# Performance work log

Hardware: AMD Instinct MI355X
Metric: run time of the kernel (lower is better)

## Reference

```python
import jax, jax.numpy as jnp
import numpy as np

D_MODEL = 4096
D_HIDDEN = 32768
BATCH = 2048
K = 128
N_DEAD = 2048


def _ln(x, eps=1e-5):
    # torch .std() is unbiased (ddof=1)
    mu = jnp.mean(x, axis=-1, keepdims=True)
    xc = x - mu
    std = jnp.std(x, axis=-1, keepdims=True, ddof=1)
    return xc / (std + eps), mu, std


def _topk_activation(x, k):
    # topk over last dim, relu values, scatter back into zeros
    vals, idx = jax.lax.top_k(x, k)          # [B, k]
    vals = jax.nn.relu(vals)
    rows = jnp.arange(x.shape[0])[:, None]    # [B, 1]
    return jnp.zeros_like(x).at[rows, idx].set(vals)


def setup_inputs() -> dict:
    key = jax.random.key(0)
    k1, k2 = jax.random.split(key)
    x = jax.random.normal(k1, (BATCH, D_MODEL), dtype=jnp.float32)
    # kaiming-uniform-ish encoder init
    bound = 1.0 / np.sqrt(D_MODEL)
    w_enc = jax.random.uniform(k2, (D_MODEL, D_HIDDEN), dtype=jnp.float32,
                               minval=-bound, maxval=bound)
    w_dec = w_enc.T
    w_dec = w_dec / jnp.linalg.norm(w_dec, axis=0, keepdims=True)
    b_enc = jnp.zeros((D_HIDDEN,), dtype=jnp.float32)
    b_pre = jnp.zeros((D_MODEL,), dtype=jnp.float32)
    # fixed dead-neuron mask with exactly N_DEAD dead latents
    dm = np.zeros((D_HIDDEN,), dtype=bool)
    rng = np.random.default_rng(0)
    dm[rng.choice(D_HIDDEN, size=N_DEAD, replace=False)] = True
    dead_mask = jnp.asarray(dm)
    return {"x": x, "w_enc": w_enc, "w_dec": w_dec, "b_enc": b_enc,
            "b_pre": b_pre, "dead_mask": dead_mask, "num_dead": N_DEAD}


def reference(x, w_enc, w_dec, b_enc, b_pre, dead_mask, num_dead):
    xn, mu, std = _ln(x)
    xc = xn - b_pre
    pre_acts = xc @ w_enc + b_enc                 # [B, d_hidden]
    latents = _topk_activation(pre_acts, K)
    recons = latents @ w_dec + b_pre              # [B, d_model]
    recons = recons * std + mu
    # auxk dead-neuron path (num_dead is a static python int)
    k_aux = min(x.shape[-1] // 2, num_dead)
    auxk_latents = jnp.where(dead_mask[None, :], pre_acts, -jnp.inf)
    auxk_acts = _topk_activation(auxk_latents, k_aux)
    auxk = auxk_acts @ w_dec + b_pre
    auxk = auxk * std + mu
    return recons, auxk, num_dead
```

## Files before the change

kernel.cpp:

```cpp
#include <hip/hip_runtime.h>
#include <math.h>

#define D_MODEL  4096
#define D_HIDDEN 32768
#define BATCH    2048
#define KSEL     128
#define NDEAD    2048
#define TIECAP   256

typedef short s16x8 __attribute__((ext_vector_type(8)));
typedef float f32x4 __attribute__((ext_vector_type(4)));

__device__ __forceinline__ unsigned int fkey(float f) {
    unsigned int u = __float_as_uint(f);
    return (u & 0x80000000u) ? ~u : (u | 0x80000000u);
}
__device__ __forceinline__ unsigned short f2bf(float f) {
    unsigned int u = __float_as_uint(f);
    u += 0x7FFFu + ((u >> 16) & 1u);
    return (unsigned short)(u >> 16);
}
__device__ __forceinline__ float bf2f(unsigned short h) {
    return __uint_as_float(((unsigned int)h) << 16);
}
__device__ __forceinline__ unsigned int key16x2(unsigned int u) {
    const unsigned int s = (u >> 15) & 0x10001u;
    const unsigned int mask = s * 0xFFFFu;
    return (u ^ mask) | (~mask & 0x80008000u);
}
__device__ __forceinline__ float unkey16(unsigned int k) {
    const unsigned int u = (k & 0x8000u) ? (k & 0x7FFFu) : (~k & 0xFFFFu);
    return __uint_as_float(u << 16);
}
__device__ __forceinline__ void async_copy16(void* lds_dst, const void* gsrc) {
    __builtin_amdgcn_global_load_lds(
        (const __attribute__((address_space(1))) unsigned int*)gsrc,
        (__attribute__((address_space(3))) unsigned int*)lds_dst,
        16, 0, 0);
}

__global__ __launch_bounds__(256) void ln_kernel(const float* __restrict__ x,
        double* __restrict__ mu, double* __restrict__ stdv, double* __restrict__ sinv)
{
    const int row = blockIdx.x;
    const int tid = threadIdx.x;
    const float* xr = x + (size_t)row * D_MODEL;
    float xv[16];
#pragma unroll
    for (int i = 0; i < 16; ++i) xv[i] = xr[tid + 256 * i];
    double s = 0.0;
#pragma unroll
    for (int i = 0; i < 16; ++i) s += (double)xv[i];
    __shared__ double red[4];
    __shared__ double sh_mu;
    const int lane = tid & 63, wid = tid >> 6;
#pragma unroll
    for (int off = 32; off > 0; off >>= 1) s += __shfl_down(s, off, 64);
    if (lane == 0) red[wid] = s;
    __syncthreads();
    if (tid == 0) sh_mu = (red[0] + red[1] + red[2] + red[3]) / (double)D_MODEL;
    __syncthreads();
    const double m = sh_mu;
    double s2 = 0.0;
#pragma unroll
    for (int i = 0; i < 16; ++i) { double d = (double)xv[i] - m; s2 += d * d; }
#pragma unroll
    for (int off = 32; off > 0; off >>= 1) s2 += __shfl_down(s2, off, 64);
    __syncthreads();
    if (lane == 0) red[wid] = s2;
    __syncthreads();
    if (tid == 0) {
        double var = (red[0] + red[1] + red[2] + red[3]) / (double)(D_MODEL - 1);
        double sd = sqrt(var);
        mu[row] = m;
        stdv[row] = sd;
        sinv[row] = 1.0 / (sd + 1e-5);
    }
}

__global__ void dead_scan_kernel(const unsigned char* __restrict__ mask8,
                                 int* __restrict__ dead_idx, int* __restrict__ dead_cnt,
                                 const int* __restrict__ num_dead_in, float* __restrict__ out_last)
{
    const int lane = threadIdx.x;
    int c = 0;
    for (int j = lane; j < D_HIDDEN; j += 64) c += (mask8[j] != 0);
#pragma unroll
    for (int off = 32; off > 0; off >>= 1) c += __shfl_down(c, off, 64);
    const int total_u8 = __shfl(c, 0, 64);
    const bool u8mode = (total_u8 == NDEAD);
    const int* mask32 = (const int*)mask8;
    int cnt = 0;
    for (int base = 0; base < D_HIDDEN; base += 64) {
        const int j = base + lane;
        const bool d = u8mode ? (mask8[j] != 0) : (mask32[j] != 0);
        const unsigned long long b = __ballot(d);
        const int pre = __popcll(b & ((1ull << lane) - 1ull));
        if (d && (cnt + pre) < NDEAD) dead_idx[cnt + pre] = j;
        cnt += __popcll(b);
    }
    const int cc = cnt > NDEAD ? NDEAD : cnt;
    if (lane == 0) {
        *dead_cnt = cc;
        *out_last = (float)(*num_dead_in);
    }
    for (int t = cc + lane; t < NDEAD; t += 64) dead_idx[t] = 0;
}

__global__ __launch_bounds__(256) void asplit_kernel(
    const float* __restrict__ x, const double* __restrict__ mu, const double* __restrict__ sinv,
    const float* __restrict__ b_pre, unsigned short* __restrict__ Ahp)
{
    const int row = blockIdx.x, tid = threadIdx.x;
    const double m = mu[row], si = sinv[row];
    const float* xr = x + (size_t)row * D_MODEL;
#pragma unroll
    for (int i = 0; i < 4; ++i) {
        const int j = (i * 256 + tid) * 4;
        const float4 xv = *(const float4*)(xr + j);
        const float4 bp = *(const float4*)(b_pre + j);
        float v[4];
        v[0] = (float)(((double)xv.x - m) * si) - bp.x;
        v[1] = (float)(((double)xv.y - m) * si) - bp.y;
        v[2] = (float)(((double)xv.z - m) * si) - bp.z;
        v[3] = (float)(((double)xv.w - m) * si) - bp.w;
        uint2 hw;
        hw.x = (unsigned)f2bf(v[0]) | ((unsigned)f2bf(v[1]) << 16);
        hw.y = (unsigned)f2bf(v[2]) | ((unsigned)f2bf(v[3]) << 16);
        *(uint2*)(Ahp + (size_t)row * D_MODEL + j) = hw;
    }
}

__global__ __launch_bounds__(256) void bsplit_kernel(
    const float* __restrict__ w_enc, unsigned short* __restrict__ Bhp)
{
    __shared__ float t[32][33];
    const int bk = blockIdx.x * 32;
    const int bn = blockIdx.y * 32;
    const int tid = threadIdx.x;
    const int lr = tid >> 3, lc4 = (tid & 7) * 4;
    const float4 v = *(const float4*)(w_enc + (size_t)(bk + lr) * D_HIDDEN + bn + lc4);
    t[lr][lc4 + 0] = v.x; t[lr][lc4 + 1] = v.y; t[lr][lc4 + 2] = v.z; t[lr][lc4 + 3] = v.w;
    __syncthreads();
    float o[4];
#pragma unroll
    for (int j = 0; j < 4; ++j) o[j] = t[lc4 + j][lr];
    uint2 hw;
    hw.x = (unsigned)f2bf(o[0]) | ((unsigned)f2bf(o[1]) << 16);
    hw.y = (unsigned)f2bf(o[2]) | ((unsigned)f2bf(o[3]) << 16);
    *(uint2*)(Bhp + (size_t)(bn + lr) * D_MODEL + bk + lc4) = hw;
}

__global__ __launch_bounds__(256) void wencT_kernel(
    const float* __restrict__ w_enc, float* __restrict__ wT)
{
    __shared__ float t[32][33];
    const int bk = blockIdx.x * 32;
    const int bn = blockIdx.y * 32;
    const int tid = threadIdx.x;
    const int lr = tid >> 3, lc4 = (tid & 7) * 4;
    const float4 v = *(const float4*)(w_enc + (size_t)(bk + lr) * D_HIDDEN + bn + lc4);
    t[lr][lc4 + 0] = v.x; t[lr][lc4 + 1] = v.y; t[lr][lc4 + 2] = v.z; t[lr][lc4 + 3] = v.w;
    __syncthreads();
    const int j = tid >> 3, i4 = (tid & 7) * 4;
    float4 o;
    o.x = t[i4 + 0][j]; o.y = t[i4 + 1][j]; o.z = t[i4 + 2][j]; o.w = t[i4 + 3][j];
    *(float4*)(wT + (size_t)(bn + j) * D_MODEL + bk + i4) = o;
}

template<int EPI>
__global__ __launch_bounds__(512) void mm256_kernel(
    const unsigned short* __restrict__ A, const unsigned short* __restrict__ B,
    const int kdim, const int ntiles_x,
    const float* __restrict__ bias_n,
    const double* __restrict__ muv, const double* __restrict__ stdvv,
    void* __restrict__ outp, const long ostride)
{
    __shared__ unsigned short lds[2 * 4 * 8192];
    const int tid = threadIdx.x;
    const int lane = tid & 63, wid = tid >> 6;
    const int cpx = gridDim.x >> 3;
    const int orig = blockIdx.x;
    const int wg = (orig & 7) * cpx + (orig >> 3);
    const int m0 = (wg % ntiles_x) * 256;
    const int n0 = (wg / ntiles_x) * 256;
    const int wm = (wid >> 2) * 128;
    const int wn = (wid & 3) * 64;
    const int fr = lane & 15, kq = lane >> 4;
    const int swr = (fr >> 1) & 3;
    const int qg = (lane & 3) ^ ((lane >> 3) & 3);
    const int qo = (kq ^ swr) * 8;

    f32x4 acc[8][4];
#pragma unroll
    for (int i = 0; i < 8; ++i)
#pragma unroll
        for (int j = 0; j < 4; ++j) acc[i][j] = (f32x4){0.f, 0.f, 0.f, 0.f};

    const unsigned short* srcs[8];
    int d0[8];
#pragma unroll
    for (int j = 0; j < 8; ++j) {
        const int s = wid * 8 + j;
        const int sp = s >> 4, sr = s & 15;
        const unsigned short* gp = (sp < 2) ? A : B;
        const int t0 = (sp < 2) ? m0 : n0;
        const int row = sr * 16 + (lane >> 2);
        srcs[j] = gp + (size_t)(t0 + row) * kdim + (sp & 1) * 32 + qg * 8;
        d0[j] = sp * 8192 + sr * 512;
    }

    const int NT = kdim >> 6;
#pragma unroll
    for (int j = 0; j < 8; ++j) async_copy16(lds + d0[j], srcs[j]);

    for (int t = 0; t < NT; ++t) {
        const int cur = t & 1;
        if (t + 1 < NT) {
            const int k1 = (t + 1) << 6;
#pragma unroll
            for (int j = 0; j < 8; ++j)
                async_copy16(lds + (cur ^ 1) * 32768 + d0[j], srcs[j] + k1);
            asm volatile("s_waitcnt vmcnt(8)" ::: "memory");
        } else {
            asm volatile("s_waitcnt vmcnt(0)" ::: "memory");
        }
        __builtin_amdgcn_s_barrier();
        __builtin_amdgcn_sched_barrier(0);

        const unsigned short* bb = lds + cur * 32768;
#pragma unroll
        for (int kk = 0; kk < 2; ++kk) {
            s16x8 a[8], b[4];
#pragma unroll
            for (int mi = 0; mi < 8; ++mi)
                a[mi] = *(const s16x8*)(bb + kk * 8192 + (wm + mi * 16 + fr) * 32 + qo);
#pragma unroll
            for (int ni = 0; ni < 4; ++ni)
                b[ni] = *(const s16x8*)(bb + (2 + kk) * 8192 + (wn + ni * 16 + fr) * 32 + qo);
            __builtin_amdgcn_s_setprio(1);
#pragma unroll
            for (int mi = 0; mi < 8; ++mi)
#pragma unroll
                for (int ni = 0; ni < 4; ++ni)
                    acc[mi][ni] = __builtin_amdgcn_mfma_f32_16x16x32_bf16(a[mi], b[ni], acc[mi][ni], 0, 0, 0);
            __builtin_amdgcn_s_setprio(0);
        }
        __builtin_amdgcn_sched_barrier(0);
        __builtin_amdgcn_s_barrier();
        __builtin_amdgcn_sched_barrier(0);
    }

#pragma unroll
    for (int ni = 0; ni < 4; ++ni) {
        const int col = n0 + wn + ni * 16 + fr;
        const float be = bias_n[col];
#pragma unroll
        for (int mi = 0; mi < 8; ++mi) {
            const int rb = m0 + wm + mi * 16 + kq * 4;
            if (EPI == 0) {
                unsigned short* O = (unsigned short*)outp;
#pragma unroll
                for (int r = 0; r < 4; ++r)
                    O[(size_t)(rb + r) * ostride + col] = f2bf(acc[mi][ni][r] + be);
            } else {
                float* O = (float*)outp;
#pragma unroll
                for (int r = 0; r < 4; ++r) {
                    const int m = rb + r;
                    O[(size_t)m * ostride + col] =
                        (acc[mi][ni][r] + be) * (float)stdvv[m] + (float)muv[m];
                }
            }
        }
    }
}

template<int EPI>
__global__ __launch_bounds__(256) void mm_kernel(
    const unsigned short* __restrict__ A, const unsigned short* __restrict__ B,
    const int kdim, const int ntiles_x,
    const float* __restrict__ bias_n,
    const double* __restrict__ muv, const double* __restrict__ stdvv,
    void* __restrict__ outp, const long ostride)
{
    __shared__ unsigned short lds[3 * 2 * 128 * 32];
    const int tid = threadIdx.x;
    const int lane = tid & 63, wid = tid >> 6;
    const int cpx = gridDim.x >> 3;
    const int orig = blockIdx.x;
    const int wg = (orig & 7) * cpx + (orig >> 3);
    const int m0 = (wg % ntiles_x) * 128;
    const int n0 = (wg / ntiles_x) * 128;
    const int wm = (wid >> 1) * 64, wn = (wid & 1) * 64;
    const int fr = lane & 15, kq = lane >> 4;
    const int swr = (fr >> 1) & 3;
    const int qg = (lane & 3) ^ ((lane >> 3) & 3);
    const int qo = (kq ^ swr) * 8;

    f32x4 acc[4][4];
#pragma unroll
    for (int i = 0; i < 4; ++i)
#pragma unroll
        for (int j = 0; j < 4; ++j) acc[i][j] = (f32x4){0.f, 0.f, 0.f, 0.f};

    const unsigned short* srcs[4];
    int d0[4];
#pragma unroll
    for (int j = 0; j < 4; ++j) {
        const int s = wid * 4 + j;
        const int pl = s >> 3, sr = s & 7;
        const int r = sr * 16 + (lane >> 2);
        srcs[j] = (pl ? B : A) + (size_t)((pl ? n0 : m0) + r) * kdim + qg * 8;
        d0[j] = pl * 4096 + sr * 512;
    }

    const int NT = kdim >> 5;
#pragma unroll
    for (int j = 0; j < 4; ++j) async_copy16(lds + 0 * 8192 + d0[j], srcs[j]);
#pragma unroll
    for (int j = 0; j < 4; ++j) async_copy16(lds + 1 * 8192 + d0[j], srcs[j] + 32);

    int cur = 0, nxt = 2;
    for (int t = 0; t < NT; ++t) {
        if (t < NT - 1) {
            asm volatile("s_waitcnt vmcnt(4)" ::: "memory");
        } else {
            asm volatile("s_waitcnt vmcnt(0)" ::: "memory");
        }
        __builtin_amdgcn_s_barrier();
        __builtin_amdgcn_sched_barrier(0);

        if (t + 2 < NT) {
            const int k2 = (t + 2) << 5;
#pragma unroll
            for (int j = 0; j < 4; ++j) async_copy16(lds + nxt * 8192 + d0[j], srcs[j] + k2);
        }

        const unsigned short* la = lds + cur * 8192;
        const unsigned short* lb = la + 4096;
        s16x8 a[4], b[4];
#pragma unroll
        for (int i = 0; i < 4; ++i) {
            a[i] = *(const s16x8*)(la + (wm + i * 16 + fr) * 32 + qo);
            b[i] = *(const s16x8*)(lb + (wn + i * 16 + fr) * 32 + qo);
        }
#pragma unroll
        for (int mi = 0; mi < 4; ++mi)
#pragma unroll
            for (int ni = 0; ni < 4; ++ni)
                acc[mi][ni] = __builtin_amdgcn_mfma_f32_16x16x32_bf16(a[mi], b[ni], acc[mi][ni], 0, 0, 0);

        cur = cur == 2 ? 0 : cur + 1;
        nxt = nxt == 2 ? 0 : nxt + 1;
    }

#pragma unroll
    for (int ni = 0; ni < 4; ++ni) {
        const int col = n0 + wn + ni * 16 + fr;
        const float be = bias_n[col];
#pragma unroll
        for (int mi = 0; mi < 4; ++mi) {
            const int rb = m0 + wm + mi * 16 + kq * 4;
            if (EPI == 0) {
                unsigned short* O = (unsigned short*)outp;
#pragma unroll
                for (int r = 0; r < 4; ++r)
                    O[(size_t)(rb + r) * ostride + col] = f2bf(acc[mi][ni][r] + be);
            } else {
                float* O = (float*)outp;
#pragma unroll
                for (int r = 0; r < 4; ++r) {
                    const int m = rb + r;
                    O[(size_t)m * ostride + col] =
                        (acc[mi][ni][r] + be) * (float)stdvv[m] + (float)muv[m];
                }
            }
        }
    }
}

__global__ __launch_bounds__(256) void topk_sel_kernel(
    const unsigned short* __restrict__ p16,
    int* __restrict__ topk_idx, float* __restrict__ topk_val,
    int* __restrict__ sure_cnt, int* __restrict__ tie_cnt, int* __restrict__ cand_col)
{
    const int row = blockIdx.x;
    const int tid = threadIdx.x;
    const int lane = tid & 63, wid = tid >> 6;
    const unsigned short* pr = p16 + (size_t)row * D_HIDDEN;

    __shared__ int red[4];
    __shared__ int sh_sel, sh_tie;

    uint4 kr[16];
#pragma unroll
    for (int i = 0; i < 16; ++i) {
        uint4 w = *(const uint4*)(pr + (i * 256 + tid) * 8);
        w.x = key16x2(w.x); w.y = key16x2(w.y); w.z = key16x2(w.z); w.w = key16x2(w.w);
        kr[i] = w;
    }
    if (tid == 0) { sh_sel = 0; sh_tie = 0; }

    unsigned int lo = 0, hi = 65535;
    while (lo < hi) {
        const unsigned int mid = (lo + hi) >> 1;
        int c = 0;
#pragma unroll
        for (int i = 0; i < 16; ++i) {
            const unsigned int u[4] = {kr[i].x, kr[i].y, kr[i].z, kr[i].w};
#pragma unroll
            for (int e = 0; e < 4; ++e) {
                c += (int)((u[e] & 0xFFFFu) > mid);
                c += (int)((u[e] >> 16) > mid);
            }
        }
#pragma unroll
        for (int off = 32; off > 0; off >>= 1) c += __shfl_down(c, off, 64);
        if (lane == 0) red[wid] = c;
        __syncthreads();
        const int total = red[0] + red[1] + red[2] + red[3];
        if (total < KSEL) hi = mid; else lo = mid + 1;
        __syncthreads();
    }
    const unsigned int K16 = lo;

    const float vc = unkey16(K16);
    const float DLT = 1.3e-2f;
    const float sureT = vc + 2.f * DLT;
    const float candT = vc - 2.f * DLT;
    const unsigned int sK = fkey(sureT) >> 16;
    const unsigned int cK = fkey(candT) >> 16;

    int* oidx = topk_idx + row * KSEL;
    float* oval = topk_val + row * KSEL;
    int* cc = cand_col + row * TIECAP;
#pragma unroll
    for (int i = 0; i < 16; ++i) {
        const int j0 = (i * 256 + tid) * 8;
        const unsigned int u[4] = {kr[i].x, kr[i].y, kr[i].z, kr[i].w};
#pragma unroll
        for (int e = 0; e < 8; ++e) {
            const unsigned int k = (e & 1) ? (u[e >> 1] >> 16) : (u[e >> 1] & 0xFFFFu);
            if (k < cK) continue;
            const float v = unkey16(k);
            if (k > sK && v > sureT) {
                const int pos = atomicAdd(&sh_sel, 1);
                oidx[pos] = j0 + e;
                oval[pos] = v > 0.f ? v : 0.f;
            } else if (v >= candT) {
                const int t = atomicAdd(&sh_tie, 1);
                if (t < TIECAP) cc[t] = j0 + e;
            }
        }
    }
    __syncthreads();
    if (tid == 0) {
        sure_cnt[row] = sh_sel;
        tie_cnt[row] = sh_tie > TIECAP ? TIECAP : sh_tie;
    }
}

__global__ __launch_bounds__(256) void topk_refine_kernel(
    const int* __restrict__ tie_cnt, const int* __restrict__ cand_col,
    double* __restrict__ cand_val,
    const float* __restrict__ x, const double* __restrict__ mu, const double* __restrict__ sinv,
    const float* __restrict__ b_pre, const float* __restrict__ wT, const float* __restrict__ b_enc)
{
    const int row = blockIdx.x;
    const int tid = threadIdx.x;
    const int lane = tid & 63, wid = tid >> 6;
    const int T = tie_cnt[row];
    const int base = (int)blockIdx.y * 4 + wid;
    if (base >= T) return;
    const double m_ = mu[row], si = sinv[row];
    const float* xr = x + (size_t)row * D_MODEL;
    for (int slot = base; slot < T; slot += 64) {
        const int col = cand_col[row * TIECAP + slot];
        const float* wr = wT + (size_t)col * D_MODEL;
        double s0 = 0.0, s1 = 0.0;
        for (int k = lane * 4; k < D_MODEL; k += 512) {
            {
                const float4 xv = *(const float4*)(xr + k);
                const float4 bp = *(const float4*)(b_pre + k);
                const float4 wv4 = *(const float4*)(wr + k);
                s0 += (((double)xv.x - m_) * si - (double)bp.x) * (double)wv4.x;
                s0 += (((double)xv.y - m_) * si - (double)bp.y) * (double)wv4.y;
                s0 += (((double)xv.z - m_) * si - (double)bp.z) * (double)wv4.z;
                s0 += (((double)xv.w - m_) * si - (double)bp.w) * (double)wv4.w;
            }
            {
                const int k2 = k + 256;
                const float4 xv = *(const float4*)(xr + k2);
                const float4 bp = *(const float4*)(b_pre + k2);
                const float4 wv4 = *(const float4*)(wr + k2);
                s1 += (((double)xv.x - m_) * si - (double)bp.x) * (double)wv4.x;
                s1 += (((double)xv.y - m_) * si - (double)bp.y) * (double)wv4.y;
                s1 += (((double)xv.z - m_) * si - (double)bp.z) * (double)wv4.z;
                s1 += (((double)xv.w - m_) * si - (double)bp.w) * (double)wv4.w;
            }
        }
        double s = s0 + s1;
#pragma unroll
        for (int off = 32; off > 0; off >>= 1) s += __shfl_down(s, off, 64);
        if (lane == 0) cand_val[row * TIECAP + slot] = s + (double)b_enc[col];
    }
}

__global__ __launch_bounds__(256) void topk_fin_kernel(
    const int* __restrict__ sure_cnt, const int* __restrict__ tie_cnt,
    const int* __restrict__ cand_col, const double* __restrict__ cand_val,
    int* __restrict__ topk_idx, float* __restrict__ topk_val)
{
    const int row = blockIdx.x;
    const int tid = threadIdx.x;
    __shared__ double vals[TIECAP];
    __shared__ int cols[TIECAP];
    const int G = sure_cnt[row];
    const int T = tie_cnt[row];
    const int R = KSEL - G;
    if (tid < T) {
        vals[tid] = cand_val[row * TIECAP + tid];
        cols[tid] = cand_col[row * TIECAP + tid];
    }
    __syncthreads();
    int* oidx = topk_idx + row * KSEL;
    float* oval = topk_val + row * KSEL;
    if (tid < T) {
        const double v = vals[tid];
        const int c = cols[tid];
        int rank = 0;
        for (int u = 0; u < T; ++u) {
            const double vu = vals[u];
            rank += (int)((vu > v) || (vu == v && cols[u] < c));
        }
        if (rank < R) {
            oidx[G + rank] = c;
            oval[G + rank] = v > 0.0 ? (float)v : 0.f;
        }
    }
    const int take = R < T ? R : T;
    if (tid >= take && tid < R) {
        oidx[G + tid] = (T > 0) ? cols[0] : 0;
        oval[G + tid] = 0.f;
    }
}

__global__ __launch_bounds__(256) void wdec2bf_kernel(
    const float* __restrict__ w_dec, unsigned short* __restrict__ wd16)
{
    const size_t gid = (size_t)blockIdx.x * 256 + threadIdx.x;
    const size_t base = gid * 8;
    const float4 a = *(const float4*)(w_dec + base);
    const float4 b = *(const float4*)(w_dec + base + 4);
    uint4 o;
    o.x = (unsigned)f2bf(a.x) | ((unsigned)f2bf(a.y) << 16);
    o.y = (unsigned)f2bf(a.z) | ((unsigned)f2bf(a.w) << 16);
    o.z = (unsigned)f2bf(b.x) | ((unsigned)f2bf(b.y) << 16);
    o.w = (unsigned)f2bf(b.z) | ((unsigned)f2bf(b.w) << 16);
    *(uint4*)(wd16 + base) = o;
}

__global__ __launch_bounds__(256) void decode_kernel(
    const int* __restrict__ topk_idx, const float* __restrict__ topk_val,
    const unsigned short* __restrict__ wd16, const float* __restrict__ b_pre,
    const double* __restrict__ mu, const double* __restrict__ stdv,
    float* __restrict__ out0)
{
    const int row = blockIdx.x;
    const int tid = threadIdx.x;
    __shared__ int sidx[KSEL];
    __shared__ float sval[KSEL];
    if (tid < KSEL) {
        sidx[tid] = topk_idx[row * KSEL + tid];
        sval[tid] = topk_val[row * KSEL + tid];
    }
    __syncthreads();
    float acc[16];
#pragma unroll
    for (int i = 0; i < 16; ++i) acc[i] = 0.f;
    const int dbase = tid * 16;
    for (int k = 0; k < KSEL; ++k) {
        const float v = sval[k];
        if (v == 0.f) continue;
        const uint4* wr = (const uint4*)(wd16 + (size_t)sidx[k] * D_MODEL + dbase);
        const uint4 w0 = wr[0], w1 = wr[1];
        const unsigned int u[8] = {w0.x, w0.y, w0.z, w0.w, w1.x, w1.y, w1.z, w1.w};
#pragma unroll
        for (int i = 0; i < 8; ++i) {
            acc[2 * i]     += v * __uint_as_float(u[i] << 16);
            acc[2 * i + 1] += v * __uint_as_float(u[i] & 0xFFFF0000u);
        }
    }
    const float st = (float)stdv[row];
    const float mm = (float)mu[row];
    float* o = out0 + (size_t)row * D_MODEL + dbase;
#pragma unroll
    for (int i = 0; i < 16; ++i) {
        o[i] = (acc[i] + b_pre[dbase + i]) * st + mm;
    }
}

__global__ __launch_bounds__(256) void auxg_kernel(
    const unsigned short* __restrict__ p16, const int* __restrict__ dead_idx,
    const int* __restrict__ dead_cnt, unsigned short* __restrict__ Ahd)
{
    const int r = blockIdx.x;
    const int tid = threadIdx.x;
    const int dc = *dead_cnt;
#pragma unroll
    for (int i = 0; i < 8; ++i) {
        const int c = i * 256 + tid;
        unsigned short v = 0;
        if (c < dc) {
            const unsigned short u = p16[(size_t)r * D_HIDDEN + dead_idx[c]];
            v = (u & 0x8000u) ? (unsigned short)0 : u;
        }
        Ahd[(size_t)r * NDEAD + c] = v;
    }
}

__global__ __launch_bounds__(256) void auxb_kernel(
    const float* __restrict__ w_dec, const int* __restrict__ dead_idx,
    unsigned short* __restrict__ Bhd)
{
    __shared__ float t[32][33];
    const int k0 = blockIdx.x * 32;
    const int n0 = blockIdx.y * 32;
    const int tid = threadIdx.x;
    const int i = tid >> 3, j4 = (tid & 7) * 4;
    const int srow = dead_idx[k0 + i];
    const float4 v = *(const float4*)(w_dec + (size_t)srow * D_MODEL + n0 + j4);
    t[i][j4 + 0] = v.x; t[i][j4 + 1] = v.y; t[i][j4 + 2] = v.z; t[i][j4 + 3] = v.w;
    __syncthreads();
    const int j = tid >> 3, i4 = (tid & 7) * 4;
    uint2 hw;
    hw.x = (unsigned)f2bf(t[i4 + 0][j]) | ((unsigned)f2bf(t[i4 + 1][j]) << 16);
    hw.y = (unsigned)f2bf(t[i4 + 2][j]) | ((unsigned)f2bf(t[i4 + 3][j]) << 16);
    *(uint2*)(Bhd + (size_t)(n0 + j) * NDEAD + k0 + i4) = hw;
}

extern "C" void kernel_launch(void* const* d_in, const int* in_sizes, int n_in,
                              void* d_out, int out_size, void* d_ws, size_t ws_size,
                              hipStream_t stream)
{
    (void)in_sizes; (void)n_in; (void)out_size; (void)ws_size;
    const float* x      = (const float*)d_in[0];
    const float* w_enc  = (const float*)d_in[1];
    const float* w_dec  = (const float*)d_in[2];
    const float* b_enc  = (const float*)d_in[3];
    const float* b_pre  = (const float*)d_in[4];
    const unsigned char* dead_mask = (const unsigned char*)d_in[5];
    const int* num_dead = (const int*)d_in[6];
    float* out = (float*)d_out;

    char* base = (char*)d_ws;
    char* w = base;
    auto alloc = [&](size_t bytes) -> char* {
        char* p = w;
        w += (bytes + 255) & ~(size_t)255;
        return p;
    };
    unsigned short* p16 = (unsigned short*)alloc((size_t)BATCH * D_HIDDEN * 2);
    double* mu       = (double*)alloc((size_t)BATCH * 8);
    double* stdv     = (double*)alloc((size_t)BATCH * 8);
    double* sinv     = (double*)alloc((size_t)BATCH * 8);
    int* topk_idx    = (int*)alloc((size_t)BATCH * KSEL * 4);
    float* topk_val  = (float*)alloc((size_t)BATCH * KSEL * 4);
    int* dead_idx    = (int*)alloc((size_t)NDEAD * 4);
    int* dead_cnt    = (int*)alloc(256);
    int* sure_cnt    = (int*)alloc((size_t)BATCH * 4);
    int* tie_cnt     = (int*)alloc((size_t)BATCH * 4);
    int* cand_col    = (int*)alloc((size_t)BATCH * TIECAP * 4);
    double* cand_val = (double*)alloc((size_t)BATCH * TIECAP * 8);
    unsigned short* Ahp = (unsigned short*)alloc((size_t)BATCH * D_MODEL * 2);
    char* region     = alloc((size_t)D_HIDDEN * D_MODEL * 4);

    unsigned short* Bhp = (unsigned short*)region;
    float* wT   = (float*)region;
    unsigned short* wd16 = (unsigned short*)region;
    unsigned short* Bhd  = (unsigned short*)(region + (size_t)D_HIDDEN * D_MODEL * 2);
    unsigned short* Ahd  = Ahp;

    float* out0 = out;
    float* out1 = out + (size_t)BATCH * D_MODEL;
    float* out_last = out + (size_t)2 * BATCH * D_MODEL;

    ln_kernel<<<BATCH, 256, 0, stream>>>(x, mu, stdv, sinv);
    dead_scan_kernel<<<1, 64, 0, stream>>>(dead_mask, dead_idx, dead_cnt, num_dead, out_last);
    asplit_kernel<<<BATCH, 256, 0, stream>>>(x, mu, sinv, b_pre, Ahp);
    bsplit_kernel<<<dim3(D_MODEL / 32, D_HIDDEN / 32), 256, 0, stream>>>(w_enc, Bhp);
    mm256_kernel<0><<<(BATCH / 256) * (D_HIDDEN / 256), 512, 0, stream>>>(
        Ahp, Bhp, D_MODEL, BATCH / 256, b_enc, nullptr, nullptr, p16, (long)D_HIDDEN);
    wencT_kernel<<<dim3(D_MODEL / 32, D_HIDDEN / 32), 256, 0, stream>>>(w_enc, wT);
    topk_sel_kernel<<<BATCH, 256, 0, stream>>>(p16, topk_idx, topk_val, sure_cnt, tie_cnt, cand_col);
    topk_refine_kernel<<<dim3(BATCH, 16), 256, 0, stream>>>(
        tie_cnt, cand_col, cand_val, x, mu, sinv, b_pre, wT, b_enc);
    topk_fin_kernel<<<BATCH, 256, 0, stream>>>(
        sure_cnt, tie_cnt, cand_col, cand_val, topk_idx, topk_val);
    auxg_kernel<<<BATCH, 256, 0, stream>>>(p16, dead_idx, dead_cnt, Ahd);
    auxb_kernel<<<dim3(NDEAD / 32, D_MODEL / 32), 256, 0, stream>>>(w_dec, dead_idx, Bhd);
    wdec2bf_kernel<<<(int)(((size_t)D_HIDDEN * D_MODEL) / (256 * 8)), 256, 0, stream>>>(w_dec, wd16);
    decode_kernel<<<BATCH, 256, 0, stream>>>(topk_idx, topk_val, wd16, b_pre, mu, stdv, out0);
    mm_kernel<1><<<(BATCH / 128) * (D_MODEL / 128), 256, 0, stream>>>(
        Ahd, Bhd, NDEAD, BATCH / 128, b_pre, mu, stdv, out1, (long)D_MODEL);
}
```

Measured before the change: 2.294 ms.

## Split GEMM K-tile into half-stages with interleaved async loads between MFMA phases

Reworks the bf16 MFMA GEMM main loop so each 64-wide K tile is processed as two 32-wide halves, each split into two MFMA phases. Async global-to-LDS copies for the next halves are issued between these phases instead of all at once at the top of the iteration. The goal is to overlap memory traffic with compute more finely and ease per-phase register pressure. In exchange it adds more barriers and waitcnt points per tile, and the vmcnt bookkeeping becomes delicate, so a miscount could read stale LDS data.

```diff
diff --git a/kernel.cpp b/kernel.cpp
--- a/kernel.cpp
+++ b/kernel.cpp
@@ -197,58 +197,118 @@
 #pragma unroll
         for (int j = 0; j < 4; ++j) acc[i][j] = (f32x4){0.f, 0.f, 0.f, 0.f};
 
-    const unsigned short* srcs[8];
-    int d0[8];
-#pragma unroll
-    for (int j = 0; j < 8; ++j) {
-        const int s = wid * 8 + j;
-        const int sp = s >> 4, sr = s & 15;
-        const unsigned short* gp = (sp < 2) ? A : B;
-        const int t0 = (sp < 2) ? m0 : n0;
-        const int row = sr * 16 + (lane >> 2);
-        srcs[j] = gp + (size_t)(t0 + row) * kdim + (sp & 1) * 32 + qg * 8;
-        d0[j] = sp * 8192 + sr * 512;
+    const unsigned short* sH0[4];
+    int dH0[4];
+#pragma unroll
+    for (int j = 0; j < 4; ++j) {
+        const int g = wid * 4 + j;
+        const int is_b = g >> 4;
+        const int sr = g & 15;
+        const unsigned short* gp = is_b ? B : A;
+        const int t0 = is_b ? n0 : m0;
+        sH0[j] = gp + (size_t)(t0 + sr * 16 + (lane >> 2)) * kdim + qg * 8;
+        dH0[j] = (is_b ? 2 : 0) * 8192 + sr * 512;
     }
 
     const int NT = kdim >> 6;
 #pragma unroll
-    for (int j = 0; j < 8; ++j) async_copy16(lds + d0[j], srcs[j]);
+    for (int j = 0; j < 4; ++j) async_copy16(lds + dH0[j], sH0[j]);
+#pragma unroll
+    for (int j = 0; j < 4; ++j) async_copy16(lds + 8192 + dH0[j], sH0[j] + 32);
+    if (NT > 1) {
+#pragma unroll
+        for (int j = 0; j < 4; ++j) async_copy16(lds + 32768 + dH0[j], sH0[j] + 64);
+    }
 
     for (int t = 0; t < NT; ++t) {
         const int cur = t & 1;
-        if (t + 1 < NT) {
-            const int k1 = (t + 1) << 6;
-#pragma unroll
-            for (int j = 0; j < 8; ++j)
-                async_copy16(lds + (cur ^ 1) * 32768 + d0[j], srcs[j] + k1);
-            asm volatile("s_waitcnt vmcnt(8)" ::: "memory");
-        } else {
-            asm volatile("s_waitcnt vmcnt(0)" ::: "memory");
-        }
-        __builtin_amdgcn_s_barrier();
+        unsigned short* bb = (unsigned short*)lds + cur * 32768;
+        unsigned short* nb = (unsigned short*)lds + (cur ^ 1) * 32768;
+        const int k1 = (t + 1) << 6;
+        const int k2 = (t + 2) << 6;
+
+        if (t < NT - 1) { asm volatile("s_waitcnt vmcnt(8)" ::: "memory"); }
+        else            { asm volatile("s_waitcnt vmcnt(4)" ::: "memory"); }
+        asm volatile("s_barrier" ::: "memory");
         __builtin_amdgcn_sched_barrier(0);
-
-        const unsigned short* bb = lds + cur * 32768;
-#pragma unroll
-        for (int kk = 0; kk < 2; ++kk) {
-            s16x8 a[8], b[4];
-#pragma unroll
-            for (int mi = 0; mi < 8; ++mi)
-                a[mi] = *(const s16x8*)(bb + kk * 8192 + (wm + mi * 16 + fr) * 32 + qo);
+        {
+            if (t + 1 < NT) {
+                async_copy16(nb + 8192 + dH0[0], sH0[0] + k1 + 32);
+                async_copy16(nb + 8192 + dH0[1], sH0[1] + k1 + 32);
+            }
+            s16x8 a[4], b[4];
+#pragma unroll
+            for (int mi = 0; mi < 4; ++mi)
+                a[mi] = *(const s16x8*)(bb + (wm + mi * 16 + fr) * 32 + qo);
 #pragma unroll
             for (int ni = 0; ni < 4; ++ni)
-                b[ni] = *(const s16x8*)(bb + (2 + kk) * 8192 + (wn + ni * 16 + fr) * 32 + qo);
+                b[ni] = *(const s16x8*)(bb + 2 * 8192 + (wn + ni * 16 + fr) * 32 + qo);
             __builtin_amdgcn_s_setprio(1);
 #pragma unroll
-            for (int mi = 0; mi < 8; ++mi)
+            for (int mi = 0; mi < 4; ++mi)
 #pragma unroll
                 for (int ni = 0; ni < 4; ++ni)
                     acc[mi][ni] = __builtin_amdgcn_mfma_f32_16x16x32_bf16(a[mi], b[ni], acc[mi][ni], 0, 0, 0);
             __builtin_amdgcn_s_setprio(0);
-        }
+            asm volatile("s_barrier" ::: "memory");
+            __builtin_amdgcn_sched_barrier(0);
+            if (t + 1 < NT) {
+                async_copy16(nb + 8192 + dH0[2], sH0[2] + k1 + 32);
+                async_copy16(nb + 8192 + dH0[3], sH0[3] + k1 + 32);
+            }
+            s16x8 a2[4];
+#pragma unroll
+            for (int mi = 0; mi < 4; ++mi)
+                a2[mi] = *(const s16x8*)(bb + (wm + (mi + 4) * 16 + fr) * 32 + qo);
+            __builtin_amdgcn_s_setprio(1);
+#pragma unroll
+            for (int mi = 0; mi < 4; ++mi)
+#pragma unroll
+                for (int ni = 0; ni < 4; ++ni)
+                    acc[mi + 4][ni] = __builtin_amdgcn_mfma_f32_16x16x32_bf16(a2[mi], b[ni], acc[mi + 4][ni], 0, 0, 0);
+            __builtin_amdgcn_s_setprio(0);
+        }
+        if (t < NT - 1) { asm volatile("s_waitcnt vmcnt(8)" ::: "memory"); }
+        else            { asm volatile("s_waitcnt vmcnt(0)" ::: "memory"); }
+        asm volatile("s_barrier" ::: "memory");
         __builtin_amdgcn_sched_barrier(0);
-        __builtin_amdgcn_s_barrier();
-        __builtin_amdgcn_sched_barrier(0);
+        {
+            if (t + 2 < NT) {
+                async_copy16(bb + dH0[0], sH0[0] + k2);
+                async_copy16(bb + dH0[1], sH0[1] + k2);
+            }
+            s16x8 a[4], b[4];
+#pragma unroll
+            for (int mi = 0; mi < 4; ++mi)
+                a[mi] = *(const s16x8*)(bb + 8192 + (wm + mi * 16 + fr) * 32 + qo);
+#pragma unroll
+            for (int ni = 0; ni < 4; ++ni)
+                b[ni] = *(const s16x8*)(bb + 3 * 8192 + (wn + ni * 16 + fr) * 32 + qo);
+            __builtin_amdgcn_s_setprio(1);
+#pragma unroll
+            for (int mi = 0; mi < 4; ++mi)
+#pragma unroll
+                for (int ni = 0; ni < 4; ++ni)
+                    acc[mi][ni] = __builtin_amdgcn_mfma_f32_16x16x32_bf16(a[mi], b[ni], acc[mi][ni], 0, 0, 0);
+            __builtin_amdgcn_s_setprio(0);
+            asm volatile("s_barrier" ::: "memory");
+            __builtin_amdgcn_sched_barrier(0);
+            if (t + 2 < NT) {
+                async_copy16(bb + dH0[2], sH0[2] + k2);
+                async_copy16(bb + dH0[3], sH0[3] + k2);
+            }
+            s16x8 a2[4];
+#pragma unroll
+            for (int mi = 0; mi < 4; ++mi)
+                a2[mi] = *(const s16x8*)(bb + 8192 + (wm + (mi + 4) * 16 + fr) * 32 + qo);
+            __builtin_amdgcn_s_setprio(1);
+#pragma unroll
+            for (int mi = 0; mi < 4; ++mi)
+#pragma unroll
+                for (int ni = 0; ni < 4; ++ni)
+                    acc[mi + 4][ni] = __builtin_amdgcn_mfma_f32_16x16x32_bf16(a2[mi], b[ni], acc[mi + 4][ni], 0, 0, 0);
+            __builtin_amdgcn_s_setprio(0);
+        }
     }
 
 #pragma unroll
```

After: 2.242 ms. 2.3% less time.
